# Performance work log

Measured on AMD Instinct MI355X. Metric: run time of the kernel, lower is better.

Reference implementation:

```python
import jax, jax.numpy as jnp
import numpy as np

K_SIZE = 2
STRIDE = 2
PAD = 0
EPS = 1e-8


def setup_inputs() -> dict:
    key = jax.random.key(0)
    # (batch, quat_groups, 4, H, W)
    x = jax.random.normal(key, (8, 64, 4, 128, 128), dtype=jnp.float32)
    return {"x": x}


def _unfold(x, k, s, p):
    """Replicates F.unfold patch extraction on (B,G,4,H,W).
    Returns (B, G, 4, k*k, L) with unfold's (kernel-row, kernel-col) ordering,
    plus H_out, W_out."""
    B, G, Q, H, W = x.shape
    xp = jnp.pad(x, ((0, 0), (0, 0), (0, 0), (p, p), (p, p)))
    Ho = (H + 2 * p - k) // s + 1
    Wo = (W + 2 * p - k) // s + 1
    patches = []
    for i in range(k):          # fixed small kernel loop (k*k = 4)
        for j in range(k):
            patches.append(xp[:, :, :, i:i + s * Ho:s, j:j + s * Wo:s])
    u = jnp.stack(patches, axis=3)            # (B,G,4,k*k,Ho,Wo)
    return u.reshape(B, G, Q, k * k, Ho * Wo), Ho, Wo


def reference(x):
    B, G, Q, H, W = x.shape
    u, Ho, Wo = _unfold(x, K_SIZE, STRIDE, PAD)     # (B,G,4,K,L)
    # per-window quaternion magnitude
    mag = jnp.sqrt(jnp.sum(u * u, axis=2))          # (B,G,K,L)
    # NOTE: faithful to source — normalization is over the L (output-position)
    # axis (dim=3), entropy summed over kernel-area axis (dim=2)
    p = mag / (jnp.sum(mag, axis=3, keepdims=True) + EPS)
    ent = -jnp.sum(p * jnp.log(p + EPS), axis=2)    # (B,G,L)
    idx = jnp.argmax(ent, axis=1)                   # (B,L), first max like torch
    # gather max-entropy quaternion group per output position
    sel = jnp.take_along_axis(u, idx[:, None, None, None, :], axis=1)[:, 0]  # (B,4,K,L)
    pooled = jnp.transpose(sel, (0, 3, 1, 2))       # (B,L,4,K) matches torch adv-index layout
    return pooled.reshape(B, -1, Ho, Wo)            # (B, 4*K, Ho, Wo), faithful quirky view
```

## Files before the change

kernel.cpp:

```cpp
#include <hip/hip_runtime.h>
#include <math.h>

#define NB 8
#define NG 64
#define NQ 4
#define NH 128
#define NW 128
#define HO 64
#define WOUT 64
#define NL 4096
#define EPSF 1e-8f

#define MAG_BYTES ((size_t)NB * NG * 4 * NL * sizeof(float))
#define S_COUNT (NB * NG * 4)

template <bool STORE_MAG>
__global__ __launch_bounds__(256) void mag_kernel(const float* __restrict__ x,
                                                  float* __restrict__ mag,
                                                  double* __restrict__ S) {
    int t = blockIdx.x * 256 + threadIdx.x;
    int wo = t & 63;
    int ho = (t >> 6) & 63;
    int g  = (t >> 12) & 63;
    int b  = t >> 18;

    const float2* xp = (const float2*)x;
    long base2 = (long)(b * NG + g) * NQ * (NH * NW / 2);

    float sq[4] = {0.f, 0.f, 0.f, 0.f};
#pragma unroll
    for (int q = 0; q < NQ; q++) {
#pragma unroll
        for (int i = 0; i < 2; i++) {
            float2 v = xp[base2 + (long)q * (NH * NW / 2) + (2 * ho + i) * (NW / 2) + wo];
            int k0 = i * 2;
            sq[k0]     = __fadd_rn(sq[k0],     __fmul_rn(v.x, v.x));
            sq[k0 + 1] = __fadd_rn(sq[k0 + 1], __fmul_rn(v.y, v.y));
        }
    }

    int l = ho * 64 + wo;
    long mbase = (long)(b * NG + g) * 4 * NL + l;
    int lane = threadIdx.x & 63;
    int sidx = (b * NG + g) * 4;
#pragma unroll
    for (int k = 0; k < 4; k++) {
        float m = __fsqrt_rn(sq[k]);
        if (STORE_MAG) mag[mbase + k * NL] = m;
        double d = (double)m;
#pragma unroll
        for (int off = 32; off; off >>= 1) d += __shfl_xor(d, off, 64);
        if (lane == k * 16) atomicAdd(&S[sidx + k], d);
    }
}

template <bool USE_MAG>
__global__ __launch_bounds__(64) void pool_kernel(const float* __restrict__ x,
                                                  const float* __restrict__ mag,
                                                  const double* __restrict__ S,
                                                  float* __restrict__ out) {
    int b = blockIdx.y;
    int l = blockIdx.x * 64 + threadIdx.x;
    int ho = l >> 6;
    int wo = l & 63;

    __shared__ float rcpS[NG * 4];
    for (int i = threadIdx.x; i < NG * 4; i += 64) {
        float denom = __fadd_rn((float)S[b * NG * 4 + i], EPSF);
        rcpS[i] = (float)(1.0 / (double)denom);
    }
    __syncthreads();

    const float* magb = mag + (long)b * NG * 4 * NL + l;
    const float2* xp = (const float2*)x;

    float best = -INFINITY;
    int bestg = 0;
    for (int g = 0; g < NG; g++) {
        float mk[4];
        if (USE_MAG) {
            const float* mg = magb + g * 4 * NL;
#pragma unroll
            for (int k = 0; k < 4; k++) mk[k] = mg[k * NL];
        } else {
            long base2 = (long)(b * NG + g) * NQ * (NH * NW / 2);
            float sq[4] = {0.f, 0.f, 0.f, 0.f};
#pragma unroll
            for (int q = 0; q < NQ; q++) {
#pragma unroll
                for (int i = 0; i < 2; i++) {
                    float2 v = xp[base2 + (long)q * (NH * NW / 2) + (2 * ho + i) * (NW / 2) + wo];
                    sq[i * 2]     = __fadd_rn(sq[i * 2],     __fmul_rn(v.x, v.x));
                    sq[i * 2 + 1] = __fadd_rn(sq[i * 2 + 1], __fmul_rn(v.y, v.y));
                }
            }
#pragma unroll
            for (int k = 0; k < 4; k++) mk[k] = __fsqrt_rn(sq[k]);
        }
        float e = 0.f;
#pragma unroll
        for (int k = 0; k < 4; k++) {
            float p = __fmul_rn(mk[k], rcpS[g * 4 + k]);
            float lg = logf(__fadd_rn(p, EPSF));
            e = __fadd_rn(e, __fmul_rn(p, lg));
        }
        e = -e;
        if (e > best) { best = e; bestg = g; }
    }

    long base2 = (long)(b * NG + bestg) * NQ * (NH * NW / 2);
    float4* o = (float4*)out + ((long)b * (NL * 16) + (long)l * 16) / 4;
#pragma unroll
    for (int q = 0; q < NQ; q++) {
        float2 t0 = xp[base2 + (long)q * (NH * NW / 2) + (2 * ho) * (NW / 2) + wo];
        float2 t1 = xp[base2 + (long)q * (NH * NW / 2) + (2 * ho + 1) * (NW / 2) + wo];
        o[q] = make_float4(t0.x, t0.y, t1.x, t1.y);
    }
}

extern "C" void kernel_launch(void* const* d_in, const int* in_sizes, int n_in,
                              void* d_out, int out_size, void* d_ws, size_t ws_size,
                              hipStream_t stream) {
    const float* x = (const float*)d_in[0];
    float* out = (float*)d_out;

    bool have_mag_ws = ws_size >= MAG_BYTES + S_COUNT * sizeof(double);

    float* mag;
    double* S;
    if (have_mag_ws) {
        mag = (float*)d_ws;
        S = (double*)((char*)d_ws + MAG_BYTES);
    } else {
        mag = nullptr;
        S = (double*)d_ws;
    }

    hipMemsetAsync(S, 0, S_COUNT * sizeof(double), stream);

    int total = NB * NG * HO * WOUT;
    int blocksA = total / 256;
    if (have_mag_ws) {
        mag_kernel<true><<<blocksA, 256, 0, stream>>>(x, mag, S);
        pool_kernel<true><<<dim3(NL / 64, NB), 64, 0, stream>>>(x, mag, S, out);
    } else {
        mag_kernel<false><<<blocksA, 256, 0, stream>>>(x, mag, S);
        pool_kernel<false><<<dim3(NL / 64, NB), 64, 0, stream>>>(x, mag, S, out);
    }
}
```

Before: 220.6 us.

## Split pooling into parallel entropy kernel with atomicMax argmax and separate gather

Replaces the per-position serial loop over 64 groups (only 512 blocks of 64 threads) with a fully parallel entropy kernel. Each thread there handles one (b,g,l) and reduces the argmax through a 64-bit atomicMax that packs an order-preserving float key with a tie-break index. A separate gather kernel then copies the winning group's patch. The mag kernel is also widened to process two output columns per thread with float4 loads and float2 stores. The change adds an extra launch, a larger memset and heavy atomic traffic, and it assumes the workspace is always large enough for mag.

```diff
diff --git a/kernel.cpp b/kernel.cpp
--- a/kernel.cpp
+++ b/kernel.cpp
@@ -6,116 +6,97 @@
 #define NQ 4
 #define NH 128
 #define NW 128
-#define HO 64
-#define WOUT 64
 #define NL 4096
 #define EPSF 1e-8f
 
-#define MAG_BYTES ((size_t)NB * NG * 4 * NL * sizeof(float))
-#define S_COUNT (NB * NG * 4)
+#define WINNER_CT (NB * NL)
+#define S_CT (NB * NG * 4)
+#define MAG_OFF ((size_t)(WINNER_CT + S_CT) * 8)
 
-template <bool STORE_MAG>
-__global__ __launch_bounds__(256) void mag_kernel(const float* __restrict__ x,
-                                                  float* __restrict__ mag,
+__global__ __launch_bounds__(256) void mag_kernel(const float4* __restrict__ x4,
+                                                  float2* __restrict__ mag2,
                                                   double* __restrict__ S) {
     int t = blockIdx.x * 256 + threadIdx.x;
-    int wo = t & 63;
-    int ho = (t >> 6) & 63;
-    int g  = (t >> 12) & 63;
-    int b  = t >> 18;
+    int wp = t & 31;
+    int ho = (t >> 5) & 63;
+    int g  = (t >> 11) & 63;
+    int b  = t >> 17;
 
-    const float2* xp = (const float2*)x;
-    long base2 = (long)(b * NG + g) * NQ * (NH * NW / 2);
-
-    float sq[4] = {0.f, 0.f, 0.f, 0.f};
+    long base4 = (long)((b * NG + g) * NQ) * (NH * NW / 4);
+    float sqA[4] = {0.f, 0.f, 0.f, 0.f};
+    float sqB[4] = {0.f, 0.f, 0.f, 0.f};
 #pragma unroll
     for (int q = 0; q < NQ; q++) {
 #pragma unroll
         for (int i = 0; i < 2; i++) {
-            float2 v = xp[base2 + (long)q * (NH * NW / 2) + (2 * ho + i) * (NW / 2) + wo];
-            int k0 = i * 2;
-            sq[k0]     = __fadd_rn(sq[k0],     __fmul_rn(v.x, v.x));
-            sq[k0 + 1] = __fadd_rn(sq[k0 + 1], __fmul_rn(v.y, v.y));
+            float4 v = x4[base4 + (long)q * (NH * NW / 4) + (2 * ho + i) * (NW / 4) + wp];
+            sqA[i * 2]     = __fadd_rn(sqA[i * 2],     __fmul_rn(v.x, v.x));
+            sqA[i * 2 + 1] = __fadd_rn(sqA[i * 2 + 1], __fmul_rn(v.y, v.y));
+            sqB[i * 2]     = __fadd_rn(sqB[i * 2],     __fmul_rn(v.z, v.z));
+            sqB[i * 2 + 1] = __fadd_rn(sqB[i * 2 + 1], __fmul_rn(v.w, v.w));
         }
     }
 
-    int l = ho * 64 + wo;
-    long mbase = (long)(b * NG + g) * 4 * NL + l;
     int lane = threadIdx.x & 63;
     int sidx = (b * NG + g) * 4;
+    long m2base = (long)sidx * (NL / 2) + ho * 32 + wp;
 #pragma unroll
     for (int k = 0; k < 4; k++) {
-        float m = __fsqrt_rn(sq[k]);
-        if (STORE_MAG) mag[mbase + k * NL] = m;
-        double d = (double)m;
+        float mA = __fsqrt_rn(sqA[k]);
+        float mB = __fsqrt_rn(sqB[k]);
+        mag2[m2base + (long)k * (NL / 2)] = make_float2(mA, mB);
+        double d = (double)mA + (double)mB;
 #pragma unroll
         for (int off = 32; off; off >>= 1) d += __shfl_xor(d, off, 64);
         if (lane == k * 16) atomicAdd(&S[sidx + k], d);
     }
 }
 
-template <bool USE_MAG>
-__global__ __launch_bounds__(64) void pool_kernel(const float* __restrict__ x,
-                                                  const float* __restrict__ mag,
+__global__ __launch_bounds__(256) void ent_kernel(const float* __restrict__ mag,
                                                   const double* __restrict__ S,
-                                                  float* __restrict__ out) {
-    int b = blockIdx.y;
-    int l = blockIdx.x * 64 + threadIdx.x;
-    int ho = l >> 6;
-    int wo = l & 63;
+                                                  unsigned long long* __restrict__ winner) {
+    int t = blockIdx.x * 256 + threadIdx.x;
+    int l = t & 4095;
+    int g = (t >> 12) & 63;
+    int b = t >> 18;
+    int sidx = (b * NG + g) * 4;
 
-    __shared__ float rcpS[NG * 4];
-    for (int i = threadIdx.x; i < NG * 4; i += 64) {
-        float denom = __fadd_rn((float)S[b * NG * 4 + i], EPSF);
-        rcpS[i] = (float)(1.0 / (double)denom);
+    __shared__ float rcp4[4];
+    if (threadIdx.x < 4) {
+        float denom = __fadd_rn((float)S[sidx + threadIdx.x], EPSF);
+        rcp4[threadIdx.x] = (float)(1.0 / (double)denom);
     }
     __syncthreads();
 
-    const float* magb = mag + (long)b * NG * 4 * NL + l;
-    const float2* xp = (const float2*)x;
+    long mbase = (long)sidx * NL + l;
+    float e = 0.f;
+#pragma unroll
+    for (int k = 0; k < 4; k++) {
+        float p = __fmul_rn(mag[mbase + (long)k * NL], rcp4[k]);
+        float lg = logf(__fadd_rn(p, EPSF));
+        e = __fadd_rn(e, __fmul_rn(p, lg));
+    }
+    float f = -e;
+    unsigned int bits = __float_as_uint(f);
+    unsigned int key = (bits & 0x80000000u) ? ~bits : (bits | 0x80000000u);
+    unsigned long long pk = ((unsigned long long)key << 32) | (unsigned long long)(63 - g);
+    atomicMax(&winner[b * NL + l], pk);
+}
 
-    float best = -INFINITY;
-    int bestg = 0;
-    for (int g = 0; g < NG; g++) {
-        float mk[4];
-        if (USE_MAG) {
-            const float* mg = magb + g * 4 * NL;
-#pragma unroll
-            for (int k = 0; k < 4; k++) mk[k] = mg[k * NL];
-        } else {
-            long base2 = (long)(b * NG + g) * NQ * (NH * NW / 2);
-            float sq[4] = {0.f, 0.f, 0.f, 0.f};
-#pragma unroll
-            for (int q = 0; q < NQ; q++) {
-#pragma unroll
-                for (int i = 0; i < 2; i++) {
-                    float2 v = xp[base2 + (long)q * (NH * NW / 2) + (2 * ho + i) * (NW / 2) + wo];
-                    sq[i * 2]     = __fadd_rn(sq[i * 2],     __fmul_rn(v.x, v.x));
-                    sq[i * 2 + 1] = __fadd_rn(sq[i * 2 + 1], __fmul_rn(v.y, v.y));
-                }
-            }
-#pragma unroll
-            for (int k = 0; k < 4; k++) mk[k] = __fsqrt_rn(sq[k]);
-        }
-        float e = 0.f;
-#pragma unroll
-        for (int k = 0; k < 4; k++) {
-            float p = __fmul_rn(mk[k], rcpS[g * 4 + k]);
-            float lg = logf(__fadd_rn(p, EPSF));
-            e = __fadd_rn(e, __fmul_rn(p, lg));
-        }
-        e = -e;
-        if (e > best) { best = e; bestg = g; }
-    }
-
-    long base2 = (long)(b * NG + bestg) * NQ * (NH * NW / 2);
-    float4* o = (float4*)out + ((long)b * (NL * 16) + (long)l * 16) / 4;
-#pragma unroll
-    for (int q = 0; q < NQ; q++) {
-        float2 t0 = xp[base2 + (long)q * (NH * NW / 2) + (2 * ho) * (NW / 2) + wo];
-        float2 t1 = xp[base2 + (long)q * (NH * NW / 2) + (2 * ho + 1) * (NW / 2) + wo];
-        o[q] = make_float4(t0.x, t0.y, t1.x, t1.y);
-    }
+__global__ __launch_bounds__(256) void gather_kernel(const float2* __restrict__ x2,
+                                                     const unsigned long long* __restrict__ winner,
+                                                     float4* __restrict__ out4) {
+    int t = blockIdx.x * 256 + threadIdx.x;
+    int q = t & 3;
+    int l = (t >> 2) & 4095;
+    int b = t >> 14;
+    unsigned long long w = winner[b * NL + l];
+    int g = 63 - (int)(w & 63ull);
+    int ho = l >> 6, wo = l & 63;
+    long base2 = (long)((b * NG + g) * NQ + q) * (NH * NW / 2);
+    float2 t0 = x2[base2 + (2 * ho) * (NW / 2) + wo];
+    float2 t1 = x2[base2 + (2 * ho + 1) * (NW / 2) + wo];
+    out4[t] = make_float4(t0.x, t0.y, t1.x, t1.y);
 }
 
 extern "C" void kernel_launch(void* const* d_in, const int* in_sizes, int n_in,
@@ -124,27 +105,15 @@
     const float* x = (const float*)d_in[0];
     float* out = (float*)d_out;
 
-    bool have_mag_ws = ws_size >= MAG_BYTES + S_COUNT * sizeof(double);
+    unsigned long long* winner = (unsigned long long*)d_ws;
+    double* S = (double*)((char*)d_ws + (size_t)WINNER_CT * 8);
+    float* mag = (float*)((char*)d_ws + MAG_OFF);
 
-    float* mag;
-    double* S;
-    if (have_mag_ws) {
-        mag = (float*)d_ws;
-        S = (double*)((char*)d_ws + MAG_BYTES);
-    } else {
-        mag = nullptr;
-        S = (double*)d_ws;
-    }
+    hipMemsetAsync(d_ws, 0, MAG_OFF, stream);
 
-    hipMemsetAsync(S, 0, S_COUNT * sizeof(double), stream);
-
-    int total = NB * NG * HO * WOUT;
-    int blocksA = total / 256;
-    if (have_mag_ws) {
-        mag_kernel<true><<<blocksA, 256, 0, stream>>>(x, mag, S);
-        pool_kernel<true><<<dim3(NL / 64, NB), 64, 0, stream>>>(x, mag, S, out);
-    } else {
-        mag_kernel<false><<<blocksA, 256, 0, stream>>>(x, mag, S);
-        pool_kernel<false><<<dim3(NL / 64, NB), 64, 0, stream>>>(x, mag, S, out);
-    }
+    mag_kernel<<<(NB * NG * 64 * 32) / 256, 256, 0, stream>>>(
+        (const float4*)x, (float2*)mag, S);
+    ent_kernel<<<(NB * NG * NL) / 256, 256, 0, stream>>>(mag, S, winner);
+    gather_kernel<<<(NB * NL * NQ) / 256, 256, 0, stream>>>(
+        (const float2*)x, winner, (float4*)out);
 }
```

New measurement: 213.0 us. -3.5%, faster.
